# Kernel tuning notes

Hardware: AMD Instinct MI355X
Metric: run time of the kernel (lower is better)

Reference implementation:

```python
import jax, jax.numpy as jnp
import numpy as np

E, DM, DH, K, DIL = 8, 512, 1024, 3, 2
N, L = 128, 128
PAD = DIL * (K - 1) // 2  # 'same' padding


def _conv1d(x, w):
    # x: [N, Cin, L], w: [Cout, Cin, K] -> [N, Cout, L]
    return jax.lax.conv_general_dilated(
        x, w, window_strides=(1,), padding=[(PAD, PAD)],
        rhs_dilation=(DIL,), dimension_numbers=("NCH", "OIH", "NCH"))


def _moe_conv(x, W, B, onehot):
    # W: [E, Cout, Cin, K], B: [E, Cout], onehot: [N, E]
    ys = jax.vmap(lambda w, b: _conv1d(x, w) + b[None, :, None])(W, B)  # [E, N, Cout, L]
    return jnp.einsum("enol,ne->nol", ys, onehot)


def setup_inputs() -> dict:
    key = jax.random.key(0)
    k1, k2, k3, k4, k5 = jax.random.split(key, 5)
    inp = jax.random.normal(k1, (N, DM, L), dtype=jnp.float32)
    # uneven per-expert sample counts summing to N (samples pre-sorted by expert)
    fwd_expert_count = jnp.asarray(np.array([10, 20, 16, 16, 12, 22, 14, 18], dtype=np.int32))
    w1 = jax.random.normal(k2, (E, DH, DM, K), dtype=jnp.float32) * 0.02
    b1 = jax.random.normal(k3, (E, DH), dtype=jnp.float32) * 0.02
    w2 = jax.random.normal(k4, (E, DM, DH, K), dtype=jnp.float32) * 0.02
    b2 = jax.random.normal(k5, (E, DM), dtype=jnp.float32) * 0.02
    return {"inp": inp, "fwd_expert_count": fwd_expert_count,
            "w1": w1, "b1": b1, "w2": w2, "b2": b2}


def reference(inp, fwd_expert_count, w1, b1, w2, b2):
    # map each sample index to its expert via cumulative counts
    cs = jnp.cumsum(fwd_expert_count)
    eid = jnp.searchsorted(cs, jnp.arange(N), side="right")  # [N]
    onehot = (eid[:, None] == jnp.arange(E)[None, :]).astype(inp.dtype)  # [N, E]
    h = _moe_conv(inp, w1, b1, onehot)       # [N, DH, L]
    h = jax.nn.gelu(h)
    out = _moe_conv(h, w2, b2, onehot)       # [N, DM, L]
    return out
```

## Files before the change

kernel.cpp:

```cpp
#include <hip/hip_runtime.h>
#include <hip/hip_bf16.h>
#include <stdint.h>


typedef __attribute__((ext_vector_type(8))) short short8;
typedef __attribute__((ext_vector_type(4))) float f32x4;

#define DMV 512
#define DHV 1024

#define OFF_X   0ull
#define OFF_H   (16ull << 20)
#define OFF_W1  (48ull << 20)
#define OFF_W2  (72ull << 20)

#define VMW(n) asm volatile("s_waitcnt vmcnt(" #n ")" ::: "memory")
#define VMNOP  do {} while (0)

__device__ __forceinline__ uint16_t f2bf(float f) {
  uint32_t u = __builtin_bit_cast(uint32_t, f);
  uint32_t r = (u + 0x7FFFu + ((u >> 16) & 1u)) >> 16;
  return (uint16_t)r;
}

__device__ __forceinline__ void async_copy16(const void* g, void* l) {
  __builtin_amdgcn_global_load_lds(
      (const __attribute__((address_space(1))) uint32_t*)g,
      (__attribute__((address_space(3))) uint32_t*)l, 16, 0, 0);
}

__device__ __forceinline__ float gelu_f(float x) {
  float u = 0.7978845608028654f * (x + 0.044715f * x * x * x);
  float t = __expf(2.0f * u);
  float th = 1.0f - 2.0f / (t + 1.0f);
  return 0.5f * x * (1.0f + th);
}

__device__ __forceinline__ void prep_x_body(uint32_t t, const float* __restrict__ inp,
                                            uint16_t* __restrict__ xp) {
  uint32_t sub = t & 3u;
  uint32_t l = (t >> 2) & 127u;
  uint32_t cc = (t >> 9) & 15u;
  uint32_t s = t >> 13;
  uint32_t fl = ((l + 2u) >> 1) & 3u;
  uint32_t c0 = cc * 32u + ((sub ^ fl) & 3u) * 8u;
  const float* src = inp + ((size_t)s * DMV + c0) * 128u + l;
  uint32_t pk[4];
#pragma unroll
  for (int p = 0; p < 4; ++p) {
    uint32_t lo = f2bf(src[(size_t)(2 * p) * 128u]);
    uint32_t hi = f2bf(src[(size_t)(2 * p + 1) * 128u]);
    pk[p] = lo | (hi << 16);
  }
  uint4 v; v.x = pk[0]; v.y = pk[1]; v.z = pk[2]; v.w = pk[3];
  ((uint4*)xp)[t] = v;
}

__device__ __forceinline__ void prep_w_body(uint32_t t, const float* __restrict__ w,
                                            uint16_t* __restrict__ wp,
                                            int C, int mtBits, int ccBits) {
  uint32_t sub = t & 3u;
  uint32_t row = (t >> 2) & 127u;
  uint32_t t2 = t >> 9;
  uint32_t k = t2 % 3u;
  uint32_t t3 = t2 / 3u;
  uint32_t mt = t3 & ((1u << mtBits) - 1u);
  uint32_t t4 = t3 >> mtBits;
  uint32_t cc = t4 & ((1u << ccBits) - 1u);
  uint32_t e = t4 >> ccBits;
  uint32_t O = 128u << mtBits;
  uint32_t o = mt * 128u + row;
  uint32_t c0 = cc * 32u + ((sub ^ (row >> 1)) & 3u) * 8u;
  const float* src = w + (((size_t)e * O + o) * (uint32_t)C + c0) * 3u + k;
  uint32_t pk[4];
#pragma unroll
  for (int p = 0; p < 4; ++p) {
    uint32_t lo = f2bf(src[(size_t)(2 * p) * 3u]);
    uint32_t hi = f2bf(src[(size_t)(2 * p + 1) * 3u]);
    pk[p] = lo | (hi << 16);
  }
  uint4 v; v.x = pk[0]; v.y = pk[1]; v.z = pk[2]; v.w = pk[3];
  ((uint4*)wp)[t] = v;
}

__global__ void prep_all(const float* __restrict__ inp,
                         const float* __restrict__ w1, const float* __restrict__ w2,
                         uint16_t* __restrict__ xp,
                         uint16_t* __restrict__ w1p, uint16_t* __restrict__ w2p) {
  uint32_t b = blockIdx.x, tid = threadIdx.x;
  if (b < 4096u)        prep_x_body(b * 256u + tid, inp, xp);
  else if (b < 10240u)  prep_w_body((b - 4096u) * 256u + tid, w1, w1p, 512, 3, 4);
  else                  prep_w_body((b - 10240u) * 256u + tid, w2, w2p, 1024, 2, 5);
}

#define PHASE_STEP(K, HH, READB, STAGE_BODY, VM_BODY)                          \
  {                                                                            \
    short8 af_[4];                                                             \
    _Pragma("unroll") for (int q = 0; q < 4; ++q)                              \
      af_[q] = *(const short8*)(br + aOff[(HH) * 4 + q] + (uint32_t)(K) * 8192u); \
    if (READB) {                                                               \
      _Pragma("unroll") for (int bq = 0; bq < 4; ++bq) {                       \
        uint32_t r_ = lB[bq] + 2u * (uint32_t)(K);                             \
        bfk[bq] = *(const short8*)(br + pOff + r_ * 64u +                      \
                    (((uint32_t)kg ^ (r_ >> 1)) & 3u) * 16u);                  \
      }                                                                        \
    }                                                                          \
    STAGE_BODY;                                                                \
    VM_BODY;                                                                   \
    __builtin_amdgcn_s_barrier();                                              \
    asm volatile("s_waitcnt lgkmcnt(0)" ::: "memory");                         \
    __builtin_amdgcn_s_setprio(1);                                             \
    _Pragma("unroll") for (int q = 0; q < 4; ++q)                              \
      _Pragma("unroll") for (int bq = 0; bq < 4; ++bq)                         \
        acc[(HH) * 4 + q][bq] = __builtin_amdgcn_mfma_f32_16x16x32_bf16(       \
            af_[q], bfk[bq], acc[(HH) * 4 + q][bq], 0, 0, 0);                  \
    __builtin_amdgcn_s_setprio(0);                                             \
    __builtin_amdgcn_s_barrier();                                              \
  }

template <int PHASE>
__global__ __launch_bounds__(512, 2) void conv_mfma(
    const uint16_t* __restrict__ bprep, const uint16_t* __restrict__ wprep,
    const float* __restrict__ bias, const int* __restrict__ cnt,
    uint16_t* __restrict__ hout, float* __restrict__ fout) {
  constexpr int CC = (PHASE == 1) ? 16 : 32;
  constexpr int HALVES = (PHASE == 1) ? 2 : 1;
  constexpr int MTP = (PHASE == 1) ? 8 : 4;
  constexpr int AREP = 4 * HALVES;
  constexpr int OO = (PHASE == 1) ? DHV : DMV;
  constexpr uint32_t AS = HALVES * 24576u;
  constexpr uint32_t BUFS = AS + 16896u;

  uint32_t b = blockIdx.x;
  uint32_t work = (b & 7u) * 32u + (b >> 3);
  const int pr = work & 63;
  const int mt = work >> 6;
  int e = 0;
  {
    int cum = cnt[0];
    while (2 * pr >= cum && e < 7) { ++e; cum += cnt[e]; }
  }
  const int tid = threadIdx.x;
  const int lane = tid & 63;
  const int wv = tid >> 6;
  const int wr = wv >> 2, wc = wv & 3;
  const int l15 = lane & 15, kg = lane >> 4;

  __shared__ __align__(16) uint8_t lds[2 * BUFS];

  uint32_t aOff[AREP];
#pragma unroll
  for (int a = 0; a < AREP; ++a) {
    uint32_t ri = (HALVES == 2) ? (uint32_t)(a * 16 + l15)
                                : (uint32_t)(wr * 64 + a * 16 + l15);
    uint32_t base = (HALVES == 2) ? (uint32_t)wr * 24576u : 0u;
    aOff[a] = base + ri * 64u + (((uint32_t)kg ^ (ri >> 1)) & 3u) * 16u;
  }
  uint32_t lB[4];
#pragma unroll
  for (int bq = 0; bq < 4; ++bq) lB[bq] = (uint32_t)((wc & 1) * 64 + bq * 16 + l15);
  const uint32_t pOff = AS + (uint32_t)(wc >> 1) * 8448u;
  const int mtBase = (PHASE == 1) ? mt * 2 : mt;

  const uint16_t* wTile0 = wprep + ((size_t)e * CC * MTP + mtBase) * 12288;
  auto SA = [&](uint8_t* bw, int ccn, int h, int k) {
    async_copy16(wTile0 + (size_t)ccn * (MTP * 12288) + (h * 3 + k) * 4096 + tid * 8,
                 bw + (uint32_t)(h * 3 + k) * 8192u + (uint32_t)tid * 16);
  };
  auto SBL = [&](uint8_t* bw, int ccn, int p) {
    async_copy16(bprep + ((size_t)(2 * pr + p) * CC + ccn) * 4096 + tid * 8,
                 bw + AS + (uint32_t)p * 8448u + 128u + (uint32_t)tid * 16);
  };

  if (tid < 64) {
    uint32_t n = (uint32_t)tid >> 5, rest = (uint32_t)tid & 31u;
    uint32_t p = rest >> 4, ri = (rest >> 2) & 3u, sb = rest & 3u;
    uint32_t rowByte = (ri < 2) ? ri * 64u : (8320u + (ri - 2) * 64u);
    uint4 z = make_uint4(0, 0, 0, 0);
    *(uint4*)(lds + n * BUFS + AS + p * 8448u + rowByte + sb * 16u) = z;
  }
  asm volatile("s_waitcnt lgkmcnt(0)" ::: "memory");

  if (PHASE == 1) {
    SBL(lds, 0, 0); SBL(lds, 0, 1);
    SA(lds, 0, 0, 0); SA(lds, 0, 1, 0);
    SA(lds, 0, 0, 1); SA(lds, 0, 1, 1);
    SA(lds, 0, 0, 2); SA(lds, 0, 1, 2);
    VMW(4);
  } else {
    SBL(lds, 0, 0); SBL(lds, 0, 1);
    SA(lds, 0, 0, 0); SA(lds, 0, 0, 1); SA(lds, 0, 0, 2);
    VMW(2);
  }
  __builtin_amdgcn_s_barrier();

  f32x4 acc[AREP][4] = {};
  short8 bfk[4];

  if (PHASE == 1) {
#pragma unroll 1
    for (int cc = 0; cc < CC - 1; ++cc) {
      const uint8_t* br = lds + (uint32_t)(cc & 1) * BUFS;
      uint8_t* bw = lds + (uint32_t)((cc & 1) ^ 1) * BUFS;
      const int cn = cc + 1;
      PHASE_STEP(0, 0, true,  { SBL(bw, cn, 0); SBL(bw, cn, 1); }, VMNOP);
      PHASE_STEP(0, 1, false, { SA(bw, cn, 0, 0); SA(bw, cn, 1, 0); }, VMW(6));
      PHASE_STEP(1, 0, true,  { SA(bw, cn, 0, 1); }, VMNOP);
      PHASE_STEP(1, 1, false, { SA(bw, cn, 1, 1); }, VMW(6));
      PHASE_STEP(2, 0, true,  { SA(bw, cn, 0, 2); }, VMNOP);
      PHASE_STEP(2, 1, false, { SA(bw, cn, 1, 2); }, VMW(4));
    }
    {
      const uint8_t* br = lds + (uint32_t)((CC - 1) & 1) * BUFS;
      PHASE_STEP(0, 0, true,  {}, VMNOP);
      PHASE_STEP(0, 1, false, {}, VMW(2));
      PHASE_STEP(1, 0, true,  {}, VMNOP);
      PHASE_STEP(1, 1, false, {}, VMW(0));
      PHASE_STEP(2, 0, true,  {}, VMNOP);
      PHASE_STEP(2, 1, false, {}, VMNOP);
    }
  } else {
#pragma unroll 1
    for (int cc = 0; cc < CC - 1; ++cc) {
      const uint8_t* br = lds + (uint32_t)(cc & 1) * BUFS;
      uint8_t* bw = lds + (uint32_t)((cc & 1) ^ 1) * BUFS;
      const int cn = cc + 1;
      PHASE_STEP(0, 0, true, { SBL(bw, cn, 0); SBL(bw, cn, 1); SA(bw, cn, 0, 0); }, VMW(4));
      PHASE_STEP(1, 0, true, { SA(bw, cn, 0, 1); }, VMW(4));
      PHASE_STEP(2, 0, true, { SA(bw, cn, 0, 2); }, VMW(2));
    }
    {
      const uint8_t* br = lds + (uint32_t)((CC - 1) & 1) * BUFS;
      PHASE_STEP(0, 0, true, {}, VMW(1));
      PHASE_STEP(1, 0, true, {}, VMW(0));
      PHASE_STEP(2, 0, true, {}, VMNOP);
    }
  }

  const int p = wc >> 1;
  const int s = 2 * pr + p;
  if (PHASE == 1) {
#pragma unroll
    for (int a = 0; a < AREP; ++a) {
      int ob = mt * 256 + wr * 128 + a * 16 + kg * 4;
      float4 bv = *(const float4*)(bias + (size_t)e * OO + ob);
      int cc2 = mt * 8 + wr * 4 + (a >> 1);
      uint32_t g = (uint32_t)((a & 1) * 2 + (kg >> 1));
      uint32_t j0 = (uint32_t)((kg & 1) * 4);
#pragma unroll
      for (int bq = 0; bq < 4; ++bq) {
        int l = (wc & 1) * 64 + bq * 16 + l15;
        uint32_t flq = ((uint32_t)(l + 2) >> 1) & 3u;
        uint32_t sub = g ^ flq;
        float v0 = gelu_f(acc[a][bq][0] + bv.x);
        float v1 = gelu_f(acc[a][bq][1] + bv.y);
        float v2 = gelu_f(acc[a][bq][2] + bv.z);
        float v3 = gelu_f(acc[a][bq][3] + bv.w);
        uint2 pk;
        pk.x = (uint32_t)f2bf(v0) | ((uint32_t)f2bf(v1) << 16);
        pk.y = (uint32_t)f2bf(v2) | ((uint32_t)f2bf(v3) << 16);
        size_t ci = ((size_t)s * 32 + cc2) * 128 + l;
        *(uint2*)(hout + ci * 32 + sub * 8 + j0) = pk;
      }
    }
  } else {
#pragma unroll
    for (int a = 0; a < AREP; ++a) {
      int ob = mt * 128 + wr * 64 + a * 16 + kg * 4;
      float4 bv = *(const float4*)(bias + (size_t)e * OO + ob);
      float bvr[4] = {bv.x, bv.y, bv.z, bv.w};
      float* op = fout + ((size_t)s * DMV + ob) * 128;
#pragma unroll
      for (int bq = 0; bq < 4; ++bq) {
        int l = (wc & 1) * 64 + bq * 16 + l15;
#pragma unroll
        for (int r = 0; r < 4; ++r)
          op[(size_t)r * 128 + l] = acc[a][bq][r] + bvr[r];
      }
    }
  }
}

extern "C" void kernel_launch(void* const* d_in, const int* in_sizes, int n_in,
                              void* d_out, int out_size, void* d_ws, size_t ws_size,
                              hipStream_t stream) {
  const float* inp = (const float*)d_in[0];
  const int* cnt = (const int*)d_in[1];
  const float* w1 = (const float*)d_in[2];
  const float* b1 = (const float*)d_in[3];
  const float* w2 = (const float*)d_in[4];
  const float* b2 = (const float*)d_in[5];
  float* out = (float*)d_out;
  uint8_t* ws = (uint8_t*)d_ws;
  uint16_t* xp = (uint16_t*)(ws + OFF_X);
  uint16_t* hp = (uint16_t*)(ws + OFF_H);
  uint16_t* w1p = (uint16_t*)(ws + OFF_W1);
  uint16_t* w2p = (uint16_t*)(ws + OFF_W2);

  prep_all<<<dim3(16384), dim3(256), 0, stream>>>(inp, w1, w2, xp, w1p, w2p);
  conv_mfma<1><<<dim3(256), dim3(512), 0, stream>>>(xp, w1p, b1, cnt, hp, nullptr);
  conv_mfma<2><<<dim3(256), dim3(512), 0, stream>>>(hp, w2p, b2, cnt, nullptr, out);
}
```

Measured before the change: 162.3 us.

## Coalesce fp32-to-bf16 prep kernels via LDS transpose and vectorized weight reads

Splits the single prep kernel into three. The input prep now stages a channel tile through LDS, reading fp32 as contiguous float4 and transposing before writing the swizzled bf16 layout. The weight prep has each thread read 12 contiguous floats (4 channels by 3 taps) as float4s and scatter them into the per-tap packed layout. Both target the strided, uncoalesced global reads of the old prep, at the cost of extra launches and narrower 8-byte scattered stores for the weights.

```diff
diff --git a/kernel.cpp b/kernel.cpp
--- a/kernel.cpp
+++ b/kernel.cpp
@@ -36,61 +36,71 @@
   return 0.5f * x * (1.0f + th);
 }
 
-__device__ __forceinline__ void prep_x_body(uint32_t t, const float* __restrict__ inp,
-                                            uint16_t* __restrict__ xp) {
-  uint32_t sub = t & 3u;
-  uint32_t l = (t >> 2) & 127u;
-  uint32_t cc = (t >> 9) & 15u;
-  uint32_t s = t >> 13;
+__global__ __launch_bounds__(256) void prep_x_t(const float* __restrict__ inp,
+                                                uint16_t* __restrict__ xp) {
+  uint32_t b = blockIdx.x;
+  uint32_t s = b >> 4, cc = b & 15u;
+  __shared__ uint16_t xs[32][132];
+  uint32_t t = threadIdx.x;
+  const float* src0 = inp + ((size_t)s * DMV + cc * 32u) * 128u;
+#pragma unroll
+  for (int i = 0; i < 4; ++i) {
+    uint32_t idx = (uint32_t)i * 256u + t;
+    uint32_t ch = idx >> 5, l4 = idx & 31u;
+    float4 f = *(const float4*)(src0 + ch * 128u + l4 * 4u);
+    uint2 pk;
+    pk.x = (uint32_t)f2bf(f.x) | ((uint32_t)f2bf(f.y) << 16);
+    pk.y = (uint32_t)f2bf(f.z) | ((uint32_t)f2bf(f.w) << 16);
+    *(uint2*)&xs[ch][l4 * 4u] = pk;
+  }
+  __syncthreads();
+  uint32_t l = t >> 1, half = t & 1u;
   uint32_t fl = ((l + 2u) >> 1) & 3u;
-  uint32_t c0 = cc * 32u + ((sub ^ fl) & 3u) * 8u;
-  const float* src = inp + ((size_t)s * DMV + c0) * 128u + l;
-  uint32_t pk[4];
-#pragma unroll
-  for (int p = 0; p < 4; ++p) {
-    uint32_t lo = f2bf(src[(size_t)(2 * p) * 128u]);
-    uint32_t hi = f2bf(src[(size_t)(2 * p + 1) * 128u]);
-    pk[p] = lo | (hi << 16);
-  }
-  uint4 v; v.x = pk[0]; v.y = pk[1]; v.z = pk[2]; v.w = pk[3];
-  ((uint4*)xp)[t] = v;
-}
-
-__device__ __forceinline__ void prep_w_body(uint32_t t, const float* __restrict__ w,
-                                            uint16_t* __restrict__ wp,
-                                            int C, int mtBits, int ccBits) {
-  uint32_t sub = t & 3u;
-  uint32_t row = (t >> 2) & 127u;
-  uint32_t t2 = t >> 9;
-  uint32_t k = t2 % 3u;
-  uint32_t t3 = t2 / 3u;
-  uint32_t mt = t3 & ((1u << mtBits) - 1u);
-  uint32_t t4 = t3 >> mtBits;
-  uint32_t cc = t4 & ((1u << ccBits) - 1u);
-  uint32_t e = t4 >> ccBits;
-  uint32_t O = 128u << mtBits;
-  uint32_t o = mt * 128u + row;
-  uint32_t c0 = cc * 32u + ((sub ^ (row >> 1)) & 3u) * 8u;
-  const float* src = w + (((size_t)e * O + o) * (uint32_t)C + c0) * 3u + k;
-  uint32_t pk[4];
-#pragma unroll
-  for (int p = 0; p < 4; ++p) {
-    uint32_t lo = f2bf(src[(size_t)(2 * p) * 3u]);
-    uint32_t hi = f2bf(src[(size_t)(2 * p + 1) * 3u]);
-    pk[p] = lo | (hi << 16);
-  }
-  uint4 v; v.x = pk[0]; v.y = pk[1]; v.z = pk[2]; v.w = pk[3];
-  ((uint4*)wp)[t] = v;
-}
-
-__global__ void prep_all(const float* __restrict__ inp,
-                         const float* __restrict__ w1, const float* __restrict__ w2,
-                         uint16_t* __restrict__ xp,
-                         uint16_t* __restrict__ w1p, uint16_t* __restrict__ w2p) {
-  uint32_t b = blockIdx.x, tid = threadIdx.x;
-  if (b < 4096u)        prep_x_body(b * 256u + tid, inp, xp);
-  else if (b < 10240u)  prep_w_body((b - 4096u) * 256u + tid, w1, w1p, 512, 3, 4);
-  else                  prep_w_body((b - 10240u) * 256u + tid, w2, w2p, 1024, 2, 5);
+#pragma unroll
+  for (int hi = 0; hi < 2; ++hi) {
+    uint32_t sub = half * 2u + (uint32_t)hi;
+    uint32_t cg = (sub ^ fl) & 3u;
+    uint32_t pk[4];
+#pragma unroll
+    for (int p2 = 0; p2 < 4; ++p2) {
+      uint32_t c0 = cg * 8u + (uint32_t)p2 * 2u;
+      pk[p2] = (uint32_t)xs[c0][l] | ((uint32_t)xs[c0 + 1][l] << 16);
+    }
+    uint4 v; v.x = pk[0]; v.y = pk[1]; v.z = pk[2]; v.w = pk[3];
+    size_t slot = (((size_t)s * 16u + cc) * 128u + l) * 4u + sub;
+    *(uint4*)(xp + slot * 8u) = v;
+  }
+}
+
+template <int LOGCG, int LOGO>
+__global__ __launch_bounds__(256) void prep_w_c(const float* __restrict__ w,
+                                                uint16_t* __restrict__ wp) {
+  constexpr uint32_t C = 4u << LOGCG;
+  constexpr uint32_t CCn = C >> 5;
+  constexpr uint32_t MTn = 1u << (LOGO - 7);
+  uint32_t t = blockIdx.x * 256u + threadIdx.x;
+  uint32_t cg = t & ((1u << LOGCG) - 1u);
+  uint32_t o = (t >> LOGCG) & ((1u << LOGO) - 1u);
+  uint32_t e = t >> (LOGCG + LOGO);
+  uint32_t row = o & 127u, mt = o >> 7;
+  const float* src = w + (((size_t)(e << LOGO) + o) * C + cg * 4u) * 3u;
+  float4 f0 = *(const float4*)(src);
+  float4 f1 = *(const float4*)(src + 4);
+  float4 f2 = *(const float4*)(src + 8);
+  uint32_t cc = cg >> 3;
+  uint32_t sub = ((cg >> 1) & 3u) ^ ((row >> 1) & 3u);
+  uint32_t j0 = (cg & 1u) * 4u;
+  size_t base = (((size_t)e * CCn + cc) * MTn + mt) * 3u;
+  uint2 q;
+  q.x = (uint32_t)f2bf(f0.x) | ((uint32_t)f2bf(f0.w) << 16);
+  q.y = (uint32_t)f2bf(f1.z) | ((uint32_t)f2bf(f2.y) << 16);
+  *(uint2*)(wp + ((base + 0u) * 128u + row) * 32u + sub * 8u + j0) = q;
+  q.x = (uint32_t)f2bf(f0.y) | ((uint32_t)f2bf(f1.x) << 16);
+  q.y = (uint32_t)f2bf(f1.w) | ((uint32_t)f2bf(f2.z) << 16);
+  *(uint2*)(wp + ((base + 1u) * 128u + row) * 32u + sub * 8u + j0) = q;
+  q.x = (uint32_t)f2bf(f0.z) | ((uint32_t)f2bf(f1.y) << 16);
+  q.y = (uint32_t)f2bf(f2.x) | ((uint32_t)f2bf(f2.w) << 16);
+  *(uint2*)(wp + ((base + 2u) * 128u + row) * 32u + sub * 8u + j0) = q;
 }
 
 #define PHASE_STEP(K, HH, READB, STAGE_BODY, VM_BODY)                          \
@@ -297,7 +307,9 @@
   uint16_t* w1p = (uint16_t*)(ws + OFF_W1);
   uint16_t* w2p = (uint16_t*)(ws + OFF_W2);
 
-  prep_all<<<dim3(16384), dim3(256), 0, stream>>>(inp, w1, w2, xp, w1p, w2p);
+  prep_x_t<<<dim3(2048), dim3(256), 0, stream>>>(inp, xp);
+  prep_w_c<7, 10><<<dim3(4096), dim3(256), 0, stream>>>(w1, w1p);
+  prep_w_c<8, 9><<<dim3(4096), dim3(256), 0, stream>>>(w2, w2p);
   conv_mfma<1><<<dim3(256), dim3(512), 0, stream>>>(xp, w1p, b1, cnt, hp, nullptr);
   conv_mfma<2><<<dim3(256), dim3(512), 0, stream>>>(hp, w2p, b2, cnt, nullptr, out);
 }
```

New measurement: 140.8 us. 1.15x faster.
